# Kernel optimization log

Hardware: AMD Instinct MI355X
Metric: run time of the kernel (lower is better)

Reference implementation:

```python
import jax, jax.numpy as jnp
import numpy as np

N_NODES, N_EDGES, D_IN, N_GRAPHS = 20000, 320000, 256, 32
H1, C1, H2, C2 = 4, 128, 4, 64


def setup_inputs() -> dict:
    key = jax.random.key(0)
    ks = jax.random.split(key, 24)
    g = lambda k, shape, fan: jax.random.normal(k, shape, jnp.float32) * (1.0 / np.sqrt(fan))
    inp = {
        'x': jax.random.normal(ks[0], (N_NODES, D_IN), jnp.float32),
        'edge_index': jax.random.randint(ks[1], (2, N_EDGES), 0, N_NODES, jnp.int32),
        'batch': jnp.sort(jax.random.randint(ks[2], (N_NODES,), 0, N_GRAPHS, jnp.int32)),
        'edge_attr': jax.random.normal(ks[3], (N_EDGES, 1), jnp.float32),
        # GATConv 1: lin [D_IN, H1*C1], att_src/dst/edge [H1,C1], lin_edge [1,H1*C1], bias [H1*C1]
        'W1': g(ks[4], (D_IN, H1 * C1), D_IN),
        'as1': g(ks[5], (H1, C1), C1),
        'ad1': g(ks[6], (H1, C1), C1),
        'We1': g(ks[7], (1, H1 * C1), 1),
        'ae1': g(ks[8], (H1, C1), C1),
        'b1': jnp.zeros((H1 * C1,), jnp.float32),
        'g1': jnp.ones((H1 * C1,), jnp.float32),
        'be1': jnp.zeros((H1 * C1,), jnp.float32),
        # GATConv 2 (concat=False -> out 64)
        'W2': g(ks[9], (H1 * C1, H2 * C2), H1 * C1),
        'as2': g(ks[10], (H2, C2), C2),
        'ad2': g(ks[11], (H2, C2), C2),
        'We2': g(ks[12], (1, H2 * C2), 1),
        'ae2': g(ks[13], (H2, C2), C2),
        'b2': jnp.zeros((C2,), jnp.float32),
        'g2': jnp.ones((C2,), jnp.float32),
        'be2': jnp.zeros((C2,), jnp.float32),
        'fw1': g(ks[14], (C2, 32), C2),
        'fb1': jnp.zeros((32,), jnp.float32),
        'fw2': g(ks[15], (32, 1), 32),
        'fb2': jnp.zeros((1,), jnp.float32),
    }
    return inp


def _gat(x, src, dst, ea, W, a_s, a_d, We, a_e, bias, H, C, concat, n):
    h = (x @ W).reshape(n, H, C)                         # [N,H,C]
    al_s = jnp.einsum('nhc,hc->nh', h, a_s)              # [N,H]
    al_d = jnp.einsum('nhc,hc->nh', h, a_d)
    e = (ea @ We).reshape(-1, H, C)                      # [E',H,C]
    al_e = jnp.einsum('ehc,hc->eh', e, a_e)
    logits = jax.nn.leaky_relu(al_s[src] + al_d[dst] + al_e, 0.2)  # [E',H]
    m = jax.ops.segment_max(logits, dst, num_segments=n)
    m = jnp.where(jnp.isfinite(m), m, 0.0)
    p = jnp.exp(logits - m[dst])
    denom = jax.ops.segment_sum(p, dst, num_segments=n)
    alpha = p / (denom[dst] + 1e-16)                     # segment softmax
    out = jax.ops.segment_sum(h[src] * alpha[:, :, None], dst, num_segments=n)
    out = out.reshape(n, H * C) if concat else out.mean(axis=1)
    return out + bias


def _bn(x, gamma, beta):
    mu = x.mean(axis=0)
    var = x.var(axis=0)
    return gamma * (x - mu) * jax.lax.rsqrt(var + 1e-5) + beta


def reference(x, edge_index, batch, edge_attr, W1, as1, ad1, We1, ae1, b1, g1, be1,
              W2, as2, ad2, We2, ae2, b2, g2, be2, fw1, fb1, fw2, fb2):
    n = x.shape[0]
    loop = jnp.arange(n, dtype=edge_index.dtype)
    src = jnp.concatenate([edge_index[0], loop])
    dst = jnp.concatenate([edge_index[1], loop])
    # self-loop edge_attr filled with mean (PyG fill_value='mean')
    ea = jnp.concatenate([edge_attr, jnp.broadcast_to(edge_attr.mean(axis=0), (n, edge_attr.shape[1]))])

    h = _gat(x, src, dst, ea, W1, as1, ad1, We1, ae1, b1, H1, C1, True, n)
    h = jax.nn.elu(_bn(h, g1, be1))
    h = _gat(h, src, dst, ea, W2, as2, ad2, We2, ae2, b2, H2, C2, False, n)
    h = jax.nn.elu(_bn(h, g2, be2))

    sums = jax.ops.segment_sum(h, batch, num_segments=N_GRAPHS)
    cnt = jax.ops.segment_sum(jnp.ones((n,), h.dtype), batch, num_segments=N_GRAPHS)
    pooled = sums / jnp.maximum(cnt, 1.0)[:, None]       # global_mean_pool
    # dropout is identity in eval mode
    out = jax.nn.elu(pooled @ fw1 + fb1) @ fw2 + fb2
    return out
```

## Files before the change

### kernel.cpp

```cpp
#include <hip/hip_runtime.h>
#include <hip/hip_bf16.h>

#define N_NODES  20000
#define MPAD     20096
#define N_EDGES  320000
#define N_EP     (N_EDGES + N_NODES)
#define D_IN     256
#define N_GRAPHS 32
#define HH1 4
#define CC1 128
#define HH2 4
#define CC2 64

#define XB_OFF      0ull
#define HB1_OFF     10289152ull
#define AGG1_OFF    30867456ull
#define HB2_OFF     51445760ull
#define OUT2A_OFF   61734912ull
#define OUT2_OFF    82214912ull
#define ALPHA_OFF   87334912ull
#define DENOM_OFF   92774912ull
#define EAF_OFF     93094912ull
#define W1BT_OFF    94374912ull
#define W2BT_OFF    94637056ull
#define CSR_OFF     94899200ull
#define ROWPTR_OFF  97619200ull
#define GSTART_OFF  97699264ull
#define SMALL_OFF   97699520ull
#define SBUF_OFF    97725120ull
#define DEG_OFF     97725184ull
#define CURS_OFF    97805184ull
#define ALS1_OFF    97885184ull
#define ALD1_OFF    98206720ull
#define ALS2_OFF    98528256ull
#define ALD2_OFF    98849792ull
#define MUSUM1_OFF  99171328ull
#define M2SUM1_OFF  99173376ull
#define MUSUM2_OFF  99175424ull
#define M2SUM2_OFF  99175936ull
#define FLAGZ_OFF   99176448ull
#define EAACC_OFF   99176576ull
#define ZERO0_START DEG_OFF
#define ZERO0_SIZE  1451456ull

#define S_AS1 0
#define S_AD1 512
#define S_WE1 1024
#define S_AE1 1536
#define S_G1  2048
#define S_BE1 2560
#define S_AS2 3072
#define S_AD2 3328
#define S_WE2 3584
#define S_AE2 3840
#define S_G2  4096
#define S_BE2 4160
#define S_FW1 4224
#define S_FB1 6272
#define S_FW2 6304
#define S_FB2 6336

typedef __attribute__((ext_vector_type(8))) short bf8_t;
typedef __attribute__((ext_vector_type(4))) float f4_t;

__global__ void detect_dtype(const unsigned short* __restrict__ xr, int* __restrict__ flag) {
    int i = blockIdx.x * blockDim.x + threadIdx.x;
    unsigned short u = xr[i];
    if ((u & 0x7F80) == 0x7F80) atomicOr(flag, 1);
}

__device__ __forceinline__ float loadF(const void* p, int i, int fp32) {
    return fp32 ? ((const float*)p)[i]
                : __bfloat162float(((const __hip_bfloat16*)p)[i]);
}

#define PB_XB  5024
#define PB_EAF 313
#define PB_W   512
#define PB_SM  16
#define PREP_BLOCKS (PB_XB + PB_EAF + 2 * PB_W + PB_SM + 1)
__global__ __launch_bounds__(256) void prep(
        const int* __restrict__ flag,
        const void* x, const void* ea, const void* W1, const void* W2,
        const void* as1, const void* ad1, const void* We1, const void* ae1,
        const void* g1, const void* be1, const void* as2, const void* ad2,
        const void* We2, const void* ae2, const void* g2, const void* be2,
        const void* fw1, const void* fb1, const void* fw2, const void* fb2,
        __hip_bfloat16* __restrict__ xb, float* __restrict__ eaf, float* __restrict__ ea_acc,
        __hip_bfloat16* __restrict__ W1bt, __hip_bfloat16* __restrict__ W2bt,
        float* __restrict__ smalls, float* __restrict__ sbuf) {
    __shared__ float sh[256];
    int b = blockIdx.x, t = threadIdx.x;
    int fp32 = flag[0];
    if (b < PB_XB) {
        int base = (b * 256 + t) * 4;
        __hip_bfloat16 tmp[4];
#pragma unroll
        for (int j = 0; j < 4; ++j) {
            int i = base + j;
            float v = (i < N_NODES * D_IN) ? loadF(x, i, fp32) : 0.f;
            tmp[j] = __float2bfloat16(v);
        }
        *(uint2*)&xb[base] = *(uint2*)tmp;
        return;
    }
    b -= PB_XB;
    if (b < PB_EAF) {
        int base = (b * 256 + t) * 4;
        float s = 0.f;
#pragma unroll
        for (int j = 0; j < 4; ++j) {
            int i = base + j;
            if (i < N_EDGES) { float v = loadF(ea, i, fp32); eaf[i] = v; s += v; }
        }
        sh[t] = s;
        __syncthreads();
        for (int st = 128; st; st >>= 1) {
            if (t < st) sh[t] += sh[t + st];
            __syncthreads();
        }
        if (t == 0) atomicAdd(ea_acc, sh[0]);
        return;
    }
    b -= PB_EAF;
    if (b < PB_W) {
        int i = b * 256 + t;
        int k = i >> 9, n = i & 511;
        W1bt[(size_t)n * 256 + k] = __float2bfloat16(loadF(W1, i, fp32));
        return;
    }
    b -= PB_W;
    if (b < PB_W) {
        int i = b * 256 + t;
        int k = i >> 8, n = i & 255;
        W2bt[(size_t)n * 512 + k] = __float2bfloat16(loadF(W2, i, fp32));
        return;
    }
    b -= PB_W;
    if (b < PB_SM) {
        const void* srcs[16] = {as1, ad1, We1, ae1, g1, be1, as2, ad2, We2, ae2, g2, be2, fw1, fb1, fw2, fb2};
        const int cnts[16] = {512, 512, 512, 512, 512, 512, 256, 256, 256, 256, 64, 64, 2048, 32, 32, 1};
        const int offs[16] = {S_AS1, S_AD1, S_WE1, S_AE1, S_G1, S_BE1, S_AS2, S_AD2,
                              S_WE2, S_AE2, S_G2, S_BE2, S_FW1, S_FB1, S_FW2, S_FB2};
        for (int i = t; i < cnts[b]; i += 256)
            smalls[offs[b] + i] = loadF(srcs[b], i, fp32);
        return;
    }
    if (t < 4) {
        float s = 0.f;
        for (int c = 0; c < CC1; ++c) s += loadF(We1, t * CC1 + c, fp32) * loadF(ae1, t * CC1 + c, fp32);
        sbuf[t] = s;
    } else if (t < 8) {
        int h = t - 4;
        float s = 0.f;
        for (int c = 0; c < CC2; ++c) s += loadF(We2, h * CC2 + c, fp32) * loadF(ae2, h * CC2 + c, fp32);
        sbuf[4 + h] = s;
    }
}

#define HIST_BLOCKS 1329
__global__ void hist_bounds(const int* __restrict__ ei, int* __restrict__ deg,
                            const int* __restrict__ batch, int* __restrict__ gstart) {
    int b = blockIdx.x, t = threadIdx.x;
    if (b < HIST_BLOCKS) {
        int e = b * 256 + t;
        if (e >= N_EP) return;
        int d = (e < N_EDGES) ? ei[N_EDGES + e] : e - N_EDGES;
        atomicAdd(&deg[d], 1);
        return;
    }
    int i = (b - HIST_BLOCKS) * 256 + t;
    if (i >= N_NODES) return;
    int bb = batch[i];
    if (i == 0) {
        for (int g = 0; g <= bb; ++g) gstart[g] = 0;
    } else {
        int pb = batch[i - 1];
        for (int g = pb + 1; g <= bb; ++g) gstart[g] = i;
    }
    if (i == N_NODES - 1) {
        for (int g = bb + 1; g <= N_GRAPHS; ++g) gstart[g] = N_NODES;
    }
}

__global__ __launch_bounds__(1024) void deg_scan(const int* __restrict__ deg, int* __restrict__ rowptr) {
    __shared__ int part[1024];
    int t = threadIdx.x;
    int lo = t * 20;
    int hi = lo + 20; if (hi > N_NODES) hi = N_NODES; if (lo > N_NODES) lo = N_NODES;
    int s = 0;
    for (int i = lo; i < hi; ++i) s += deg[i];
    part[t] = s;
    __syncthreads();
    for (int off = 1; off < 1024; off <<= 1) {
        int u = (t >= off) ? part[t - off] : 0;
        __syncthreads();
        if (t >= off) part[t] += u;
        __syncthreads();
    }
    int run = part[t] - s;
    for (int i = lo; i < hi; ++i) { rowptr[i] = run; run += deg[i]; }
    if (hi == N_NODES && lo < N_NODES) rowptr[N_NODES] = run;
}

__global__ void edge_scatter(const int* __restrict__ ei, const int* __restrict__ rowptr,
                             int* __restrict__ cursor, int2* __restrict__ csr_se) {
    int e = blockIdx.x * blockDim.x + threadIdx.x;
    if (e >= N_EP) return;
    int s, d;
    if (e < N_EDGES) { s = ei[e]; d = ei[N_EDGES + e]; }
    else { s = d = e - N_EDGES; }
    int pos = rowptr[d] + atomicAdd(&cursor[d], 1);
    csr_se[pos] = make_int2(s, e);
}

__global__ __launch_bounds__(256) void gemm_mfma_al(
        const short* __restrict__ A, const short* __restrict__ Bt,
        __hip_bfloat16* __restrict__ Cb, int N, int K,
        float* __restrict__ als, float* __restrict__ ald,
        const float* __restrict__ asv, const float* __restrict__ adv, int cshift) {
    __shared__ short As[128 * 40];
    __shared__ short Bs[64 * 40];
    int t = threadIdx.x;
    int wv = t >> 6, lane = t & 63, quad = lane >> 4, lr = lane & 15;
    int m0 = blockIdx.y * 128, n0 = blockIdx.x * 64;
    f4_t acc[2][4] = {};
    int ra0 = t >> 2, sa0 = t & 3;
    int ra1 = (t + 256) >> 2;
    for (int k0 = 0; k0 < K; k0 += 32) {
        *(uint4*)&As[ra0 * 40 + sa0 * 8] = *(const uint4*)&A[(size_t)(m0 + ra0) * K + k0 + sa0 * 8];
        *(uint4*)&As[ra1 * 40 + sa0 * 8] = *(const uint4*)&A[(size_t)(m0 + ra1) * K + k0 + sa0 * 8];
        *(uint4*)&Bs[ra0 * 40 + sa0 * 8] = *(const uint4*)&Bt[(size_t)(n0 + ra0) * K + k0 + sa0 * 8];
        __syncthreads();
        bf8_t a0 = *(const bf8_t*)&As[(wv * 16 + lr) * 40 + quad * 8];
        bf8_t a1 = *(const bf8_t*)&As[((wv + 4) * 16 + lr) * 40 + quad * 8];
#pragma unroll
        for (int nt = 0; nt < 4; ++nt) {
            bf8_t b = *(const bf8_t*)&Bs[(nt * 16 + lr) * 40 + quad * 8];
            acc[0][nt] = __builtin_amdgcn_mfma_f32_16x16x32_bf16(a0, b, acc[0][nt], 0, 0, 0);
            acc[1][nt] = __builtin_amdgcn_mfma_f32_16x16x32_bf16(a1, b, acc[1][nt], 0, 0, 0);
        }
        __syncthreads();
    }
#pragma unroll
    for (int si = 0; si < 2; ++si) {
        int mrow = m0 + (wv + si * 4) * 16 + quad * 4;
#pragma unroll
        for (int nt = 0; nt < 4; ++nt) {
            int col = n0 + nt * 16 + lr;
#pragma unroll
            for (int r = 0; r < 4; ++r)
                Cb[(size_t)(mrow + r) * N + col] = __float2bfloat16(acc[si][nt][r]);
        }
    }
    float asv4[4], adv4[4];
#pragma unroll
    for (int nt = 0; nt < 4; ++nt) {
        asv4[nt] = asv[n0 + nt * 16 + lr];
        adv4[nt] = adv[n0 + nt * 16 + lr];
    }
    int hsel = n0 >> cshift;
#pragma unroll
    for (int si = 0; si < 2; ++si) {
#pragma unroll
        for (int r = 0; r < 4; ++r) {
            float ps = 0.f, pd = 0.f;
#pragma unroll
            for (int nt = 0; nt < 4; ++nt) {
                ps += acc[si][nt][r] * asv4[nt];
                pd += acc[si][nt][r] * adv4[nt];
            }
#pragma unroll
            for (int m = 1; m < 16; m <<= 1) {
                ps += __shfl_xor(ps, m);
                pd += __shfl_xor(pd, m);
            }
            if (lr == 0) {
                int row = m0 + (wv + si * 4) * 16 + quad * 4 + r;
                atomicAdd(&als[row * 4 + hsel], ps);
                atomicAdd(&ald[row * 4 + hsel], pd);
            }
        }
    }
}

__global__ __launch_bounds__(64) void edge_softmax_csr(
        const int* __restrict__ rowptr, const int2* __restrict__ csr_se,
        const float* __restrict__ als, const float* __restrict__ ald,
        const float* __restrict__ eaf, const float* __restrict__ ea_acc,
        const float* __restrict__ sbuf, float* __restrict__ alpha, float* __restrict__ denom) {
    int d = blockIdx.x;
    int lane = threadIdx.x;
    int beg = rowptr[d], end = rowptr[d + 1];
    float ea_mean = ea_acc[0] * (1.0f / N_EDGES);
    float4 ad = *(const float4*)&ald[d * 4];
    float s0 = sbuf[0], s1 = sbuf[1], s2 = sbuf[2], s3 = sbuf[3];
    float m0 = -INFINITY, m1 = -INFINITY, m2 = -INFINITY, m3 = -INFINITY;
    for (int p = beg + lane; p < end; p += 64) {
        int2 se = csr_se[p];
        float eav = (se.y < N_EDGES) ? eaf[se.y] : ea_mean;
        float4 as = *(const float4*)&als[se.x * 4];
        float l0 = as.x + ad.x + eav * s0; l0 = l0 > 0.f ? l0 : 0.2f * l0;
        float l1 = as.y + ad.y + eav * s1; l1 = l1 > 0.f ? l1 : 0.2f * l1;
        float l2 = as.z + ad.z + eav * s2; l2 = l2 > 0.f ? l2 : 0.2f * l2;
        float l3 = as.w + ad.w + eav * s3; l3 = l3 > 0.f ? l3 : 0.2f * l3;
        float4 lv = {l0, l1, l2, l3};
        *(float4*)&alpha[(size_t)p * 4] = lv;
        m0 = fmaxf(m0, l0); m1 = fmaxf(m1, l1); m2 = fmaxf(m2, l2); m3 = fmaxf(m3, l3);
    }
#pragma unroll
    for (int off = 1; off < 64; off <<= 1) {
        m0 = fmaxf(m0, __shfl_xor(m0, off));
        m1 = fmaxf(m1, __shfl_xor(m1, off));
        m2 = fmaxf(m2, __shfl_xor(m2, off));
        m3 = fmaxf(m3, __shfl_xor(m3, off));
    }
    float t0 = 0.f, t1 = 0.f, t2 = 0.f, t3 = 0.f;
    for (int p = beg + lane; p < end; p += 64) {
        float4 lv = *(const float4*)&alpha[(size_t)p * 4];
        lv.x = __expf(lv.x - m0); lv.y = __expf(lv.y - m1);
        lv.z = __expf(lv.z - m2); lv.w = __expf(lv.w - m3);
        *(float4*)&alpha[(size_t)p * 4] = lv;
        t0 += lv.x; t1 += lv.y; t2 += lv.z; t3 += lv.w;
    }
#pragma unroll
    for (int off = 1; off < 64; off <<= 1) {
        t0 += __shfl_xor(t0, off);
        t1 += __shfl_xor(t1, off);
        t2 += __shfl_xor(t2, off);
        t3 += __shfl_xor(t3, off);
    }
    if (lane == 0) {
        float4 dn = {t0, t1, t2, t3};
        *(float4*)&denom[d * 4] = dn;
    }
}

template <int HC, int C, bool B16OUT>
__global__ __launch_bounds__(HC / 4) void agg_csr_bf(
        const int* __restrict__ rowptr, const int2* __restrict__ csr_se,
        const float* __restrict__ alpha, const float* __restrict__ denom,
        const __hip_bfloat16* __restrict__ hb, void* __restrict__ outb) {
    int d = blockIdx.x;
    int t = threadIdx.x;
    int h = (4 * t) / C;
    float rdn = 1.0f / (denom[d * (HC / C) + h] + 1e-16f);
    float a0 = 0.f, a1 = 0.f, a2 = 0.f, a3 = 0.f;
    int beg = rowptr[d], end = rowptr[d + 1];
    for (int p = beg; p < end; ++p) {
        int2 se = csr_se[p];
        float w = alpha[(size_t)p * 4 + h];
        uint2 raw = *(const uint2*)&hb[(size_t)se.x * HC + 4 * t];
        a0 += w * __uint_as_float(raw.x << 16);
        a1 += w * __uint_as_float(raw.x & 0xFFFF0000u);
        a2 += w * __uint_as_float(raw.y << 16);
        a3 += w * __uint_as_float(raw.y & 0xFFFF0000u);
    }
    a0 *= rdn; a1 *= rdn; a2 *= rdn; a3 *= rdn;
    if (B16OUT) {
        __hip_bfloat16 tmp[4] = {__float2bfloat16(a0), __float2bfloat16(a1),
                                 __float2bfloat16(a2), __float2bfloat16(a3)};
        *(uint2*)&((__hip_bfloat16*)outb)[(size_t)d * HC + 4 * t] = *(uint2*)tmp;
    } else {
        float4 v = {a0, a1, a2, a3};
        *(float4*)&((float*)outb)[(size_t)d * HC + 4 * t] = v;
    }
}

__global__ __launch_bounds__(256) void bn_part_b(const __hip_bfloat16* __restrict__ x,
                                                 float* __restrict__ musum, float* __restrict__ m2sum) {
    int t = threadIdx.x;
    float s0 = 0.f, s20 = 0.f, s1 = 0.f, s21 = 0.f;
    for (int i = blockIdx.x; i < N_NODES; i += gridDim.x) {
        unsigned u = *(const unsigned*)&x[(size_t)i * 512 + 2 * t];
        float v0 = __uint_as_float(u << 16);
        float v1 = __uint_as_float(u & 0xFFFF0000u);
        s0 += v0; s20 += v0 * v0; s1 += v1; s21 += v1 * v1;
    }
    atomicAdd(&musum[2 * t], s0);
    atomicAdd(&m2sum[2 * t], s20);
    atomicAdd(&musum[2 * t + 1], s1);
    atomicAdd(&m2sum[2 * t + 1], s21);
}

__global__ __launch_bounds__(256) void bn_apply_elu_b16(__hip_bfloat16* __restrict__ x,
                                                        const float* __restrict__ musum,
                                                        const float* __restrict__ m2sum,
                                                        const float* __restrict__ smalls) {
    int q = blockIdx.x * blockDim.x + threadIdx.x;
    if (q >= N_NODES * 512 / 4) return;
    int base = q * 4;
    int j = base & 511;
    uint2 raw = *(uint2*)&x[base];
    float v[4] = {__uint_as_float(raw.x << 16), __uint_as_float(raw.x & 0xFFFF0000u),
                  __uint_as_float(raw.y << 16), __uint_as_float(raw.y & 0xFFFF0000u)};
    __hip_bfloat16 tmp[4];
#pragma unroll
    for (int k = 0; k < 4; ++k) {
        int jj = j + k;
        float m = musum[jj] * (1.0f / N_NODES);
        float var = m2sum[jj] * (1.0f / N_NODES) - m * m;
        float y = smalls[S_G1 + jj] * (v[k] - m) * rsqrtf(var + 1e-5f) + smalls[S_BE1 + jj];
        y = y > 0.f ? y : expm1f(y);
        tmp[k] = __float2bfloat16(y);
    }
    *(uint2*)&x[base] = *(uint2*)tmp;
}

__global__ __launch_bounds__(256) void head_mean_stats(const float* __restrict__ ina, float* __restrict__ outb,
                                                       float* __restrict__ musum, float* __restrict__ m2sum) {
    int t = threadIdx.x;
    int c = t & 63, j = t >> 6;
    float ls = 0.f, ls2 = 0.f;
    for (int nd = blockIdx.x * 4 + j; nd < N_NODES; nd += gridDim.x * 4) {
        size_t base = (size_t)nd * 256 + c;
        float s = (ina[base] + ina[base + 64] + ina[base + 128] + ina[base + 192]) * 0.25f;
        outb[(size_t)nd * 64 + c] = s;
        ls += s; ls2 += s * s;
    }
    __shared__ float shs[4][64], sh2[4][64];
    shs[j][c] = ls; sh2[j][c] = ls2;
    __syncthreads();
    if (j == 0) {
        atomicAdd(&musum[c], shs[0][c] + shs[1][c] + shs[2][c] + shs[3][c]);
        atomicAdd(&m2sum[c], sh2[0][c] + sh2[1][c] + sh2[2][c] + sh2[3][c]);
    }
}

__global__ void bn_apply_elu_f32(float* __restrict__ x, const float* __restrict__ musum,
                                 const float* __restrict__ m2sum, const float* __restrict__ smalls) {
    int i = blockIdx.x * blockDim.x + threadIdx.x;
    if (i >= N_NODES * 64) return;
    int j = i & 63;
    float m = musum[j] * (1.0f / N_NODES);
    float var = m2sum[j] * (1.0f / N_NODES) - m * m;
    float y = smalls[S_G2 + j] * (x[i] - m) * rsqrtf(var + 1e-5f) + smalls[S_BE2 + j];
    x[i] = y > 0.f ? y : expm1f(y);
}

__global__ __launch_bounds__(256) void pool_mlp(const float* __restrict__ x, const int* __restrict__ gstart,
                                                const float* __restrict__ smalls, const int* __restrict__ flag,
                                                void* __restrict__ outp) {
    int g = blockIdx.x;
    int t = threadIdx.x;
    int c = t & 63, j = t >> 6;
    int beg = gstart[g], end = gstart[g + 1];
    float s = 0.f;
    for (int i = beg + j; i < end; i += 4)
        s += x[(size_t)i * 64 + c];
    __shared__ float sh[4][64];
    __shared__ float pooled[64];
    __shared__ float hsh[32];
    sh[j][c] = s;
    __syncthreads();
    if (j == 0) {
        float tot = sh[0][c] + sh[1][c] + sh[2][c] + sh[3][c];
        pooled[c] = tot / fmaxf((float)(end - beg), 1.0f);
    }
    __syncthreads();
    if (t < 32) {
        float acc = smalls[S_FB1 + t];
        for (int cc = 0; cc < 64; ++cc)
            acc += pooled[cc] * smalls[S_FW1 + cc * 32 + t];
        hsh[t] = acc > 0.f ? acc : expm1f(acc);
    }
    __syncthreads();
    if (t == 0) {
        float o = smalls[S_FB2];
        for (int k = 0; k < 32; ++k) o += hsh[k] * smalls[S_FW2 + k];
        if (flag[0]) ((float*)outp)[g] = o;
        else ((__hip_bfloat16*)outp)[g] = __float2bfloat16(o);
    }
}

extern "C" void kernel_launch(void* const* d_in, const int* in_sizes, int n_in,
                              void* d_out, int out_size, void* d_ws, size_t ws_size,
                              hipStream_t stream) {
    const void* x    = d_in[0];
    const int* ei    = (const int*)d_in[1];
    const int* batch = (const int*)d_in[2];
    const void* ea   = d_in[3];
    const void* W1   = d_in[4];
    const void* as1  = d_in[5];
    const void* ad1  = d_in[6];
    const void* We1  = d_in[7];
    const void* ae1  = d_in[8];
    const void* g1   = d_in[10];
    const void* be1  = d_in[11];
    const void* W2   = d_in[12];
    const void* as2  = d_in[13];
    const void* ad2  = d_in[14];
    const void* We2  = d_in[15];
    const void* ae2  = d_in[16];
    const void* g2   = d_in[18];
    const void* be2  = d_in[19];
    const void* fw1  = d_in[20];
    const void* fb1  = d_in[21];
    const void* fw2  = d_in[22];
    const void* fb2  = d_in[23];

    char* ws = (char*)d_ws;
    __hip_bfloat16* xb   = (__hip_bfloat16*)(ws + XB_OFF);
    __hip_bfloat16* hb1  = (__hip_bfloat16*)(ws + HB1_OFF);
    __hip_bfloat16* agg1 = (__hip_bfloat16*)(ws + AGG1_OFF);
    __hip_bfloat16* hb2  = (__hip_bfloat16*)(ws + HB2_OFF);
    float* out2a  = (float*)(ws + OUT2A_OFF);
    float* out2   = (float*)(ws + OUT2_OFF);
    float* alpha  = (float*)(ws + ALPHA_OFF);
    float* denom  = (float*)(ws + DENOM_OFF);
    float* eaf    = (float*)(ws + EAF_OFF);
    __hip_bfloat16* W1bt = (__hip_bfloat16*)(ws + W1BT_OFF);
    __hip_bfloat16* W2bt = (__hip_bfloat16*)(ws + W2BT_OFF);
    int2*  csr_se = (int2*)(ws + CSR_OFF);
    int*   rowptr = (int*)(ws + ROWPTR_OFF);
    int*   gstart = (int*)(ws + GSTART_OFF);
    float* smalls = (float*)(ws + SMALL_OFF);
    float* sbuf   = (float*)(ws + SBUF_OFF);
    int*   deg    = (int*)(ws + DEG_OFF);
    int*   cursor = (int*)(ws + CURS_OFF);
    float* als1   = (float*)(ws + ALS1_OFF);
    float* ald1   = (float*)(ws + ALD1_OFF);
    float* als2   = (float*)(ws + ALS2_OFF);
    float* ald2   = (float*)(ws + ALD2_OFF);
    float* musum1 = (float*)(ws + MUSUM1_OFF);
    float* m2sum1 = (float*)(ws + M2SUM1_OFF);
    float* musum2 = (float*)(ws + MUSUM2_OFF);
    float* m2sum2 = (float*)(ws + M2SUM2_OFF);
    int*   flag   = (int*)(ws + FLAGZ_OFF);
    float* ea_acc = (float*)(ws + EAACC_OFF);

    hipMemsetAsync(ws + ZERO0_START, 0, ZERO0_SIZE, stream);
    hipMemsetAsync(ws + AGG1_OFF + (size_t)N_NODES * 512 * 2, 0, (MPAD - N_NODES) * 512 * 2, stream);

    detect_dtype<<<256, 256, 0, stream>>>((const unsigned short*)x, flag);
    prep<<<PREP_BLOCKS, 256, 0, stream>>>(flag, x, ea, W1, W2,
                                          as1, ad1, We1, ae1, g1, be1, as2, ad2,
                                          We2, ae2, g2, be2, fw1, fb1, fw2, fb2,
                                          xb, eaf, ea_acc, W1bt, W2bt, smalls, sbuf);

    hist_bounds<<<HIST_BLOCKS + 79, 256, 0, stream>>>(ei, deg, batch, gstart);
    deg_scan<<<1, 1024, 0, stream>>>(deg, rowptr);
    edge_scatter<<<HIST_BLOCKS, 256, 0, stream>>>(ei, rowptr, cursor, csr_se);

    gemm_mfma_al<<<dim3(512 / 64, MPAD / 128), 256, 0, stream>>>(
        (const short*)xb, (const short*)W1bt, hb1, 512, 256,
        als1, ald1, smalls + S_AS1, smalls + S_AD1, 7);
    edge_softmax_csr<<<N_NODES, 64, 0, stream>>>(rowptr, csr_se, als1, ald1, eaf, ea_acc, sbuf, alpha, denom);
    agg_csr_bf<512, 128, true><<<N_NODES, 128, 0, stream>>>(rowptr, csr_se, alpha, denom, hb1, agg1);
    bn_part_b<<<256, 256, 0, stream>>>(agg1, musum1, m2sum1);
    bn_apply_elu_b16<<<10000, 256, 0, stream>>>(agg1, musum1, m2sum1, smalls);

    gemm_mfma_al<<<dim3(256 / 64, MPAD / 128), 256, 0, stream>>>(
        (const short*)agg1, (const short*)W2bt, hb2, 256, 512,
        als2, ald2, smalls + S_AS2, smalls + S_AD2, 6);
    edge_softmax_csr<<<N_NODES, 64, 0, stream>>>(rowptr, csr_se, als2, ald2, eaf, ea_acc, sbuf + 4, alpha, denom);
    agg_csr_bf<256, 64, false><<<N_NODES, 64, 0, stream>>>(rowptr, csr_se, alpha, denom, hb2, out2a);
    head_mean_stats<<<256, 256, 0, stream>>>(out2a, out2, musum2, m2sum2);
    bn_apply_elu_f32<<<(N_NODES * 64 + 255) / 256, 256, 0, stream>>>(out2, musum2, m2sum2, smalls);

    pool_mlp<<<N_GRAPHS, 256, 0, stream>>>(out2, gstart, smalls, flag, d_out);
}
```

Baseline: 496.3 us.

## Make reductions deterministic and fuse head-mean into layer-2 aggregation

Float atomics in the edge_attr sum, the attention-logit projections and the batch-norm statistics are replaced by per-block partial buffers plus small reduction kernels, and a per-node CSR sort orders edges by id. This gives a deterministic summation order. The layer-2 head mean moves into the aggregation kernel, which drops the 256-wide fp32 intermediate and its extra read/write pass. In exchange it adds several small launches and a serial insertion sort per node, which costs time on high-degree nodes.

```diff
diff --git a/kernel.cpp b/kernel.cpp
--- a/kernel.cpp
+++ b/kernel.cpp
@@ -16,32 +16,38 @@
 #define HB1_OFF     10289152ull
 #define AGG1_OFF    30867456ull
 #define HB2_OFF     51445760ull
-#define OUT2A_OFF   61734912ull
-#define OUT2_OFF    82214912ull
-#define ALPHA_OFF   87334912ull
-#define DENOM_OFF   92774912ull
-#define EAF_OFF     93094912ull
-#define W1BT_OFF    94374912ull
-#define W2BT_OFF    94637056ull
-#define CSR_OFF     94899200ull
-#define ROWPTR_OFF  97619200ull
-#define GSTART_OFF  97699264ull
-#define SMALL_OFF   97699520ull
-#define SBUF_OFF    97725120ull
-#define DEG_OFF     97725184ull
-#define CURS_OFF    97805184ull
-#define ALS1_OFF    97885184ull
-#define ALD1_OFF    98206720ull
-#define ALS2_OFF    98528256ull
-#define ALD2_OFF    98849792ull
-#define MUSUM1_OFF  99171328ull
-#define M2SUM1_OFF  99173376ull
-#define MUSUM2_OFF  99175424ull
-#define M2SUM2_OFF  99175936ull
-#define FLAGZ_OFF   99176448ull
-#define EAACC_OFF   99176576ull
+#define OUT2_OFF    61734912ull
+#define ALPHA_OFF   66854912ull
+#define DENOM_OFF   72294912ull
+#define EAF_OFF     72614912ull
+#define W1BT_OFF    73894912ull
+#define W2BT_OFF    74157056ull
+#define CSR_OFF     74419200ull
+#define ROWPTR_OFF  77139200ull
+#define GSTART_OFF  77219264ull
+#define SMALL_OFF   77219520ull
+#define SBUF_OFF    77245120ull
+#define EAP_OFF     77245184ull
+#define ALSP_OFF    77246464ull
+#define ALDP_OFF    77889536ull
+#define ALS1_OFF    78532608ull
+#define ALD1_OFF    78854144ull
+#define ALS2_OFF    79175680ull
+#define ALD2_OFF    79497216ull
+#define PMU1_OFF    79818752ull
+#define PM21_OFF    80343040ull
+#define PMU2_OFF    80867328ull
+#define PM22_OFF    80932864ull
+#define MUSUM1_OFF  80998400ull
+#define M2SUM1_OFF  81000448ull
+#define MUSUM2_OFF  81002496ull
+#define M2SUM2_OFF  81003008ull
+#define EAACC_OFF   81003520ull
+#define DEG_OFF     81003584ull
+#define CURS_OFF    81083584ull
+#define FLAGZ_OFF   81163584ull
 #define ZERO0_START DEG_OFF
-#define ZERO0_SIZE  1451456ull
+#define ZERO0_SIZE  160128ull
 
 #define S_AS1 0
 #define S_AD1 512
@@ -86,7 +92,7 @@
         const void* g1, const void* be1, const void* as2, const void* ad2,
         const void* We2, const void* ae2, const void* g2, const void* be2,
         const void* fw1, const void* fb1, const void* fw2, const void* fb2,
-        __hip_bfloat16* __restrict__ xb, float* __restrict__ eaf, float* __restrict__ ea_acc,
+        __hip_bfloat16* __restrict__ xb, float* __restrict__ eaf, float* __restrict__ eap,
         __hip_bfloat16* __restrict__ W1bt, __hip_bfloat16* __restrict__ W2bt,
         float* __restrict__ smalls, float* __restrict__ sbuf) {
     __shared__ float sh[256];
@@ -119,7 +125,7 @@
             if (t < st) sh[t] += sh[t + st];
             __syncthreads();
         }
-        if (t == 0) atomicAdd(ea_acc, sh[0]);
+        if (t == 0) eap[b] = sh[0];
         return;
     }
     b -= PB_EAF;
@@ -183,7 +189,8 @@
     }
 }
 
-__global__ __launch_bounds__(1024) void deg_scan(const int* __restrict__ deg, int* __restrict__ rowptr) {
+__global__ __launch_bounds__(1024) void deg_scan(const int* __restrict__ deg, int* __restrict__ rowptr,
+                                                 const float* __restrict__ eap, float* __restrict__ ea_acc) {
     __shared__ int part[1024];
     int t = threadIdx.x;
     int lo = t * 20;
@@ -201,6 +208,11 @@
     int run = part[t] - s;
     for (int i = lo; i < hi; ++i) { rowptr[i] = run; run += deg[i]; }
     if (hi == N_NODES && lo < N_NODES) rowptr[N_NODES] = run;
+    if (t == 0) {
+        float es = 0.f;
+        for (int i = 0; i < PB_EAF; ++i) es += eap[i];
+        ea_acc[0] = es;
+    }
 }
 
 __global__ void edge_scatter(const int* __restrict__ ei, const int* __restrict__ rowptr,
@@ -214,10 +226,37 @@
     csr_se[pos] = make_int2(s, e);
 }
 
+__global__ __launch_bounds__(64) void csr_sort(const int* __restrict__ rowptr, int2* __restrict__ cs) {
+    __shared__ int2 buf[128];
+    int d = blockIdx.x;
+    int beg = rowptr[d], end = rowptr[d + 1], n = end - beg;
+    int lane = threadIdx.x;
+    if (n <= 1) return;
+    if (n <= 128) {
+        for (int i = lane; i < n; i += 64) buf[i] = cs[beg + i];
+        __syncthreads();
+        if (lane == 0) {
+            for (int i = 1; i < n; ++i) {
+                int2 key = buf[i]; int j = i - 1;
+                while (j >= 0 && buf[j].y > key.y) { buf[j + 1] = buf[j]; --j; }
+                buf[j + 1] = key;
+            }
+        }
+        __syncthreads();
+        for (int i = lane; i < n; i += 64) cs[beg + i] = buf[i];
+    } else if (lane == 0) {
+        for (int i = beg + 1; i < end; ++i) {
+            int2 key = cs[i]; int j = i - 1;
+            while (j >= beg && cs[j].y > key.y) { cs[j + 1] = cs[j]; --j; }
+            cs[j + 1] = key;
+        }
+    }
+}
+
 __global__ __launch_bounds__(256) void gemm_mfma_al(
         const short* __restrict__ A, const short* __restrict__ Bt,
         __hip_bfloat16* __restrict__ Cb, int N, int K,
-        float* __restrict__ als, float* __restrict__ ald,
+        float* __restrict__ alsp, float* __restrict__ aldp,
         const float* __restrict__ asv, const float* __restrict__ adv, int cshift) {
     __shared__ short As[128 * 40];
     __shared__ short Bs[64 * 40];
@@ -260,6 +299,7 @@
         adv4[nt] = adv[n0 + nt * 16 + lr];
     }
     int hsel = n0 >> cshift;
+    int parity = (n0 >> 6) & ((1 << (cshift - 6)) - 1);
 #pragma unroll
     for (int si = 0; si < 2; ++si) {
 #pragma unroll
@@ -277,11 +317,20 @@
             }
             if (lr == 0) {
                 int row = m0 + (wv + si * 4) * 16 + quad * 4 + r;
-                atomicAdd(&als[row * 4 + hsel], ps);
-                atomicAdd(&ald[row * 4 + hsel], pd);
+                alsp[(row * 4 + hsel) * 2 + parity] = ps;
+                aldp[(row * 4 + hsel) * 2 + parity] = pd;
             }
         }
     }
+}
+
+__global__ void al_combine(const float* __restrict__ alsp, const float* __restrict__ aldp,
+                           float* __restrict__ als, float* __restrict__ ald, int nparts) {
+    int i = blockIdx.x * blockDim.x + threadIdx.x;
+    if (i >= MPAD * 4) return;
+    float s = alsp[2 * i], d0 = aldp[2 * i];
+    if (nparts == 2) { s += alsp[2 * i + 1]; d0 += aldp[2 * i + 1]; }
+    als[i] = s; ald[i] = d0;
 }
 
 __global__ __launch_bounds__(64) void edge_softmax_csr(
@@ -336,51 +385,84 @@
     }
 }
 
-template <int HC, int C, bool B16OUT>
-__global__ __launch_bounds__(HC / 4) void agg_csr_bf(
+__global__ __launch_bounds__(128) void agg1_csr(
         const int* __restrict__ rowptr, const int2* __restrict__ csr_se,
         const float* __restrict__ alpha, const float* __restrict__ denom,
-        const __hip_bfloat16* __restrict__ hb, void* __restrict__ outb) {
+        const __hip_bfloat16* __restrict__ hb, __hip_bfloat16* __restrict__ outb) {
     int d = blockIdx.x;
     int t = threadIdx.x;
-    int h = (4 * t) / C;
-    float rdn = 1.0f / (denom[d * (HC / C) + h] + 1e-16f);
+    int h = t >> 5;
+    float rdn = 1.0f / (denom[d * 4 + h] + 1e-16f);
     float a0 = 0.f, a1 = 0.f, a2 = 0.f, a3 = 0.f;
     int beg = rowptr[d], end = rowptr[d + 1];
     for (int p = beg; p < end; ++p) {
         int2 se = csr_se[p];
         float w = alpha[(size_t)p * 4 + h];
-        uint2 raw = *(const uint2*)&hb[(size_t)se.x * HC + 4 * t];
+        uint2 raw = *(const uint2*)&hb[(size_t)se.x * 512 + 4 * t];
         a0 += w * __uint_as_float(raw.x << 16);
         a1 += w * __uint_as_float(raw.x & 0xFFFF0000u);
         a2 += w * __uint_as_float(raw.y << 16);
         a3 += w * __uint_as_float(raw.y & 0xFFFF0000u);
     }
-    a0 *= rdn; a1 *= rdn; a2 *= rdn; a3 *= rdn;
-    if (B16OUT) {
-        __hip_bfloat16 tmp[4] = {__float2bfloat16(a0), __float2bfloat16(a1),
-                                 __float2bfloat16(a2), __float2bfloat16(a3)};
-        *(uint2*)&((__hip_bfloat16*)outb)[(size_t)d * HC + 4 * t] = *(uint2*)tmp;
-    } else {
-        float4 v = {a0, a1, a2, a3};
-        *(float4*)&((float*)outb)[(size_t)d * HC + 4 * t] = v;
+    __hip_bfloat16 tmp[4] = {__float2bfloat16(a0 * rdn), __float2bfloat16(a1 * rdn),
+                             __float2bfloat16(a2 * rdn), __float2bfloat16(a3 * rdn)};
+    *(uint2*)&outb[(size_t)d * 512 + 4 * t] = *(uint2*)tmp;
+}
+
+__global__ __launch_bounds__(64) void agg2_hm(
+        const int* __restrict__ rowptr, const int2* __restrict__ csr_se,
+        const float* __restrict__ alpha, const float* __restrict__ denom,
+        const __hip_bfloat16* __restrict__ hb, float* __restrict__ out2) {
+    int d = blockIdx.x;
+    int t = threadIdx.x;
+    int h = t >> 4;
+    float rdn = 1.0f / (denom[d * 4 + h] + 1e-16f);
+    float a0 = 0.f, a1 = 0.f, a2 = 0.f, a3 = 0.f;
+    int beg = rowptr[d], end = rowptr[d + 1];
+    for (int p = beg; p < end; ++p) {
+        int2 se = csr_se[p];
+        float w = alpha[(size_t)p * 4 + h];
+        uint2 raw = *(const uint2*)&hb[(size_t)se.x * 256 + 4 * t];
+        a0 += w * __uint_as_float(raw.x << 16);
+        a1 += w * __uint_as_float(raw.x & 0xFFFF0000u);
+        a2 += w * __uint_as_float(raw.y << 16);
+        a3 += w * __uint_as_float(raw.y & 0xFFFF0000u);
+    }
+    __shared__ float sh[256];
+    sh[4 * t] = a0 * rdn; sh[4 * t + 1] = a1 * rdn;
+    sh[4 * t + 2] = a2 * rdn; sh[4 * t + 3] = a3 * rdn;
+    __syncthreads();
+    if (t < 16) {
+        float4 v;
+        v.x = 0.25f * (sh[4 * t] + sh[64 + 4 * t] + sh[128 + 4 * t] + sh[192 + 4 * t]);
+        v.y = 0.25f * (sh[4 * t + 1] + sh[64 + 4 * t + 1] + sh[128 + 4 * t + 1] + sh[192 + 4 * t + 1]);
+        v.z = 0.25f * (sh[4 * t + 2] + sh[64 + 4 * t + 2] + sh[128 + 4 * t + 2] + sh[192 + 4 * t + 2]);
+        v.w = 0.25f * (sh[4 * t + 3] + sh[64 + 4 * t + 3] + sh[128 + 4 * t + 3] + sh[192 + 4 * t + 3]);
+        *(float4*)&out2[(size_t)d * 64 + 4 * t] = v;
     }
 }
 
 __global__ __launch_bounds__(256) void bn_part_b(const __hip_bfloat16* __restrict__ x,
-                                                 float* __restrict__ musum, float* __restrict__ m2sum) {
-    int t = threadIdx.x;
+                                                 float* __restrict__ pmu, float* __restrict__ pm2) {
+    int t = threadIdx.x, b = blockIdx.x;
     float s0 = 0.f, s20 = 0.f, s1 = 0.f, s21 = 0.f;
-    for (int i = blockIdx.x; i < N_NODES; i += gridDim.x) {
+    for (int i = b; i < N_NODES; i += gridDim.x) {
         unsigned u = *(const unsigned*)&x[(size_t)i * 512 + 2 * t];
         float v0 = __uint_as_float(u << 16);
         float v1 = __uint_as_float(u & 0xFFFF0000u);
         s0 += v0; s20 += v0 * v0; s1 += v1; s21 += v1 * v1;
     }
-    atomicAdd(&musum[2 * t], s0);
-    atomicAdd(&m2sum[2 * t], s20);
-    atomicAdd(&musum[2 * t + 1], s1);
-    atomicAdd(&m2sum[2 * t + 1], s21);
+    pmu[b * 512 + 2 * t] = s0;     pm2[b * 512 + 2 * t] = s20;
+    pmu[b * 512 + 2 * t + 1] = s1; pm2[b * 512 + 2 * t + 1] = s21;
+}
+
+__global__ void bn_reduce(const float* __restrict__ pmu, const float* __restrict__ pm2,
+                          float* __restrict__ musum, float* __restrict__ m2sum, int nch) {
+    int c = blockIdx.x * blockDim.x + threadIdx.x;
+    if (c >= nch) return;
+    float s = 0.f, s2 = 0.f;
+    for (int b = 0; b < 256; ++b) { s += pmu[b * nch + c]; s2 += pm2[b * nch + c]; }
+    musum[c] = s; m2sum[c] = s2;
 }
 
 __global__ __launch_bounds__(256) void bn_apply_elu_b16(__hip_bfloat16* __restrict__ x,
@@ -398,32 +480,30 @@
 #pragma unroll
     for (int k = 0; k < 4; ++k) {
         int jj = j + k;
-        float m = musum[jj] * (1.0f / N_NODES);
-        float var = m2sum[jj] * (1.0f / N_NODES) - m * m;
-        float y = smalls[S_G1 + jj] * (v[k] - m) * rsqrtf(var + 1e-5f) + smalls[S_BE1 + jj];
+        float mm = musum[jj] * (1.0f / N_NODES);
+        float var = m2sum[jj] * (1.0f / N_NODES) - mm * mm;
+        float y = smalls[S_G1 + jj] * (v[k] - mm) * rsqrtf(var + 1e-5f) + smalls[S_BE1 + jj];
         y = y > 0.f ? y : expm1f(y);
         tmp[k] = __float2bfloat16(y);
     }
     *(uint2*)&x[base] = *(uint2*)tmp;
 }
 
-__global__ __launch_bounds__(256) void head_mean_stats(const float* __restrict__ ina, float* __restrict__ outb,
-                                                       float* __restrict__ musum, float* __restrict__ m2sum) {
+__global__ __launch_bounds__(256) void bn2_stats(const float* __restrict__ x,
+                                                 float* __restrict__ pmu, float* __restrict__ pm2) {
     int t = threadIdx.x;
     int c = t & 63, j = t >> 6;
     float ls = 0.f, ls2 = 0.f;
     for (int nd = blockIdx.x * 4 + j; nd < N_NODES; nd += gridDim.x * 4) {
-        size_t base = (size_t)nd * 256 + c;
-        float s = (ina[base] + ina[base + 64] + ina[base + 128] + ina[base + 192]) * 0.25f;
-        outb[(size_t)nd * 64 + c] = s;
-        ls += s; ls2 += s * s;
+        float v = x[(size_t)nd * 64 + c];
+        ls += v; ls2 += v * v;
     }
     __shared__ float shs[4][64], sh2[4][64];
     shs[j][c] = ls; sh2[j][c] = ls2;
     __syncthreads();
     if (j == 0) {
-        atomicAdd(&musum[c], shs[0][c] + shs[1][c] + shs[2][c] + shs[3][c]);
-        atomicAdd(&m2sum[c], sh2[0][c] + sh2[1][c] + sh2[2][c] + sh2[3][c]);
+        pmu[blockIdx.x * 64 + c] = shs[0][c] + shs[1][c] + shs[2][c] + shs[3][c];
+        pm2[blockIdx.x * 64 + c] = sh2[0][c] + sh2[1][c] + sh2[2][c] + sh2[3][c];
     }
 }
 
@@ -504,7 +584,6 @@
     __hip_bfloat16* hb1  = (__hip_bfloat16*)(ws + HB1_OFF);
     __hip_bfloat16* agg1 = (__hip_bfloat16*)(ws + AGG1_OFF);
     __hip_bfloat16* hb2  = (__hip_bfloat16*)(ws + HB2_OFF);
-    float* out2a  = (float*)(ws + OUT2A_OFF);
     float* out2   = (float*)(ws + OUT2_OFF);
     float* alpha  = (float*)(ws + ALPHA_OFF);
     float* denom  = (float*)(ws + DENOM_OFF);
@@ -516,18 +595,25 @@
     int*   gstart = (int*)(ws + GSTART_OFF);
     float* smalls = (float*)(ws + SMALL_OFF);
     float* sbuf   = (float*)(ws + SBUF_OFF);
-    int*   deg    = (int*)(ws + DEG_OFF);
-    int*   cursor = (int*)(ws + CURS_OFF);
+    float* eap    = (float*)(ws + EAP_OFF);
+    float* alsp   = (float*)(ws + ALSP_OFF);
+    float* aldp   = (float*)(ws + ALDP_OFF);
     float* als1   = (float*)(ws + ALS1_OFF);
     float* ald1   = (float*)(ws + ALD1_OFF);
     float* als2   = (float*)(ws + ALS2_OFF);
     float* ald2   = (float*)(ws + ALD2_OFF);
+    float* pmu1   = (float*)(ws + PMU1_OFF);
+    float* pm21   = (float*)(ws + PM21_OFF);
+    float* pmu2   = (float*)(ws + PMU2_OFF);
+    float* pm22   = (float*)(ws + PM22_OFF);
     float* musum1 = (float*)(ws + MUSUM1_OFF);
     float* m2sum1 = (float*)(ws + M2SUM1_OFF);
     float* musum2 = (float*)(ws + MUSUM2_OFF);
     float* m2sum2 = (float*)(ws + M2SUM2_OFF);
+    float* ea_acc = (float*)(ws + EAACC_OFF);
+    int*   deg    = (int*)(ws + DEG_OFF);
+    int*   cursor = (int*)(ws + CURS_OFF);
     int*   flag   = (int*)(ws + FLAGZ_OFF);
-    float* ea_acc = (float*)(ws + EAACC_OFF);
 
     hipMemsetAsync(ws + ZERO0_START, 0, ZERO0_SIZE, stream);
     hipMemsetAsync(ws + AGG1_OFF + (size_t)N_NODES * 512 * 2, 0, (MPAD - N_NODES) * 512 * 2, stream);
@@ -536,26 +622,31 @@
     prep<<<PREP_BLOCKS, 256, 0, stream>>>(flag, x, ea, W1, W2,
                                           as1, ad1, We1, ae1, g1, be1, as2, ad2,
                                           We2, ae2, g2, be2, fw1, fb1, fw2, fb2,
-                                          xb, eaf, ea_acc, W1bt, W2bt, smalls, sbuf);
+                                          xb, eaf, eap, W1bt, W2bt, smalls, sbuf);
 
     hist_bounds<<<HIST_BLOCKS + 79, 256, 0, stream>>>(ei, deg, batch, gstart);
-    deg_scan<<<1, 1024, 0, stream>>>(deg, rowptr);
+    deg_scan<<<1, 1024, 0, stream>>>(deg, rowptr, eap, ea_acc);
     edge_scatter<<<HIST_BLOCKS, 256, 0, stream>>>(ei, rowptr, cursor, csr_se);
+    csr_sort<<<N_NODES, 64, 0, stream>>>(rowptr, csr_se);
 
     gemm_mfma_al<<<dim3(512 / 64, MPAD / 128), 256, 0, stream>>>(
         (const short*)xb, (const short*)W1bt, hb1, 512, 256,
-        als1, ald1, smalls + S_AS1, smalls + S_AD1, 7);
+        alsp, aldp, smalls + S_AS1, smalls + S_AD1, 7);
+    al_combine<<<(MPAD * 4 + 255) / 256, 256, 0, stream>>>(alsp, aldp, als1, ald1, 2);
     edge_softmax_csr<<<N_NODES, 64, 0, stream>>>(rowptr, csr_se, als1, ald1, eaf, ea_acc, sbuf, alpha, denom);
-    agg_csr_bf<512, 128, true><<<N_NODES, 128, 0, stream>>>(rowptr, csr_se, alpha, denom, hb1, agg1);
-    bn_part_b<<<256, 256, 0, stream>>>(agg1, musum1, m2sum1);
+    agg1_csr<<<N_NODES, 128, 0, stream>>>(rowptr, csr_se, alpha, denom, hb1, agg1);
+    bn_part_b<<<256, 256, 0, stream>>>(agg1, pmu1, pm21);
+    bn_reduce<<<2, 256, 0, stream>>>(pmu1, pm21, musum1, m2sum1, 512);
     bn_apply_elu_b16<<<10000, 256, 0, stream>>>(agg1, musum1, m2sum1, smalls);
 
     gemm_mfma_al<<<dim3(256 / 64, MPAD / 128), 256, 0, stream>>>(
         (const short*)agg1, (const short*)W2bt, hb2, 256, 512,
-        als2, ald2, smalls + S_AS2, smalls + S_AD2, 6);
+        alsp, aldp, smalls + S_AS2, smalls + S_AD2, 6);
+    al_combine<<<(MPAD * 4 + 255) / 256, 256, 0, stream>>>(alsp, aldp, als2, ald2, 1);
     edge_softmax_csr<<<N_NODES, 64, 0, stream>>>(rowptr, csr_se, als2, ald2, eaf, ea_acc, sbuf + 4, alpha, denom);
-    agg_csr_bf<256, 64, false><<<N_NODES, 64, 0, stream>>>(rowptr, csr_se, alpha, denom, hb2, out2a);
-    head_mean_stats<<<256, 256, 0, stream>>>(out2a, out2, musum2, m2sum2);
+    agg2_hm<<<N_NODES, 64, 0, stream>>>(rowptr, csr_se, alpha, denom, hb2, out2);
+    bn2_stats<<<256, 256, 0, stream>>>(out2, pmu2, pm22);
+    bn_reduce<<<1, 256, 0, stream>>>(pmu2, pm22, musum2, m2sum2, 64);
     bn_apply_elu_f32<<<(N_NODES * 64 + 255) / 256, 256, 0, stream>>>(out2, musum2, m2sum2, smalls);
 
     pool_mlp<<<N_GRAPHS, 256, 0, stream>>>(out2, gstart, smalls, flag, d_out);
```

Measured after the change: 520.8 us. 1.05x slower.
